# Optimization experiments

Measured on AMD Instinct MI355X. Metric: run time of the kernel, lower is better.

Reference implementation:

```python
import jax, jax.numpy as jnp
import numpy as np

# (multiplicity, dim=2l+1) per irreducible field, for both input and output
RS = [(8, 1), (8, 3), (8, 5)]
SIZE = 3          # conv kernel spatial size
B_EL = 2          # radial basis elements per (i,j) kernel block
EPS = 1e-5


def _se3_bn_conv(x, weight, bases):
    """Training-mode SE3BatchNorm stats fused into dynamic kernel build + conv3d.
    x: (B, C_in, D, H, W); weight: flat (sum mi*mj*b_el,);
    bases[i][j]: (b_el, di, dj, SIZE, SIZE, SIZE).
    """
    B = x.shape[0]
    means = []    # per scalar (d==1) field: (m,)
    scales = []   # per field: (m,) inverse-std factors
    ix = 0
    for m, d in RS:
        field = x[:, ix:ix + m * d].reshape(B, m, d, -1)
        ix += m * d
        if d == 1:
            mean = jax.lax.stop_gradient(field.mean(axis=-1).mean(axis=0).reshape(-1))
            field = field - mean.reshape(1, m, 1, 1)
            means.append(mean)
        # reduce='mean': sum over d, mean over spatial, mean over batch (detached)
        norm = jax.lax.stop_gradient(jnp.sum(field * field, axis=2).mean(axis=-1).mean(axis=0))
        scales.append((norm + EPS) ** -0.5)

    # Build normalized dynamic kernel blocks and compensating bias
    widx = 0
    row_blocks = []
    bias_parts = []
    for i, (mi, di) in enumerate(RS):
        col_blocks = []
        bia = jnp.zeros((mi * di,), x.dtype)
        imean = 0
        for j, (mj, dj) in enumerate(RS):
            basis = bases[i][j]                     # (b, di, dj, s, s, s)
            b = basis.shape[0]
            w = weight[widx:widx + mi * mj * b].reshape(mi, mj, b)
            widx += mi * mj * b
            w = w * scales[j][None, :, None]        # per-input-field BN rescale
            # block: (mi*di, mj*dj, s, s, s)
            block = jnp.einsum('uvb,bdexyz->udvexyz', w, basis)
            col_blocks.append(block.reshape(mi * di, mj * dj, SIZE, SIZE, SIZE))
            if di == 1 and dj == 1:
                mean = means[imean]
                imean += 1
                identity = basis.reshape(b, -1).sum(-1)         # (b,)
                corr = (w.reshape(-1, b) @ identity[:, None]).reshape(mi, mj)
                bia = bia - (corr @ mean[:, None]).reshape(-1)
        row_blocks.append(jnp.concatenate(col_blocks, axis=1))
        bias_parts.append(bia)
    kernel = jnp.concatenate(row_blocks, axis=0)    # (C_out, C_in, s, s, s)
    bias = jnp.concatenate(bias_parts)              # (C_out,)

    out = jax.lax.conv_general_dilated(
        x, kernel, window_strides=(1, 1, 1), padding='VALID',
        dimension_numbers=('NCDHW', 'OIDHW', 'NCDHW'))
    return out + bias[None, :, None, None, None]


def setup_inputs() -> dict:
    key = jax.random.key(0)
    k_x, k_w = jax.random.split(key)
    C = sum(m * d for m, d in RS)  # 72
    x = jax.random.normal(k_x, (8, C, 32, 32, 32), jnp.float32)
    total_w = sum(mi * mj * B_EL for mi, _ in RS for mj, _ in RS)  # 1152
    weight = jax.random.normal(k_w, (total_w,), jnp.float32) * 0.1
    inp = {'x': x, 'weight': weight}
    for i, (mi, di) in enumerate(RS):
        for j, (mj, dj) in enumerate(RS):
            kb = jax.random.fold_in(key, 100 + 10 * i + j)
            inp['basis_{}_{}'.format(i, j)] = jax.random.normal(
                kb, (B_EL, di, dj, SIZE, SIZE, SIZE), jnp.float32) / (SIZE ** 1.5)
    return inp


def reference(x, weight, basis_0_0, basis_0_1, basis_0_2,
              basis_1_0, basis_1_1, basis_1_2,
              basis_2_0, basis_2_1, basis_2_2):
    bases = [[basis_0_0, basis_0_1, basis_0_2],
             [basis_1_0, basis_1_1, basis_1_2],
             [basis_2_0, basis_2_1, basis_2_2]]
    return _se3_bn_conv(x, weight, bases)
```

## Files before the change

### kernel.cpp

```cpp
#include <hip/hip_runtime.h>
#include <hip/hip_fp16.h>
#include <math.h>

#define NCH 72
#define SP  32768
#define NBATCH 8
#define NTOT (NBATCH*SP)

#define WS_SUMX   0
#define WS_SUMSQ  72
#define WS_SCALE  144
#define WS_BIAS   216
#define WS_K      288

#define WS_XH_BYTES 323712
#define XH_ROW   2720
#define XH_PLANE 87040
#define XH_BATCH 2785280

typedef __attribute__((ext_vector_type(8))) _Float16 half8;
typedef __attribute__((ext_vector_type(4))) float float4v;
typedef __attribute__((ext_vector_type(4))) int int4v;

__device__ __forceinline__ void chmap(int c, int& f, int& m, int& d, int& dim) {
  if (c < 8)       { f = 0; m = c;          d = 0;          dim = 1; }
  else if (c < 32) { f = 1; m = (c - 8)/3;  d = (c - 8)%3;  dim = 3; }
  else             { f = 2; m = (c - 32)/5; d = (c - 32)%5; dim = 5; }
}

__global__ __launch_bounds__(256) void prepack_kernel(const float* __restrict__ x,
                                                      float* __restrict__ ws) {
  __shared__ __align__(16) short tile[256 * 88];
  __shared__ float segS[72][3], segQ[72][3];
  const int t    = threadIdx.x;
  const int z    = blockIdx.x >> 1;
  const int half = blockIdx.x & 1;
  const int b    = blockIdx.y;
  ushort* xh = (ushort*)((char*)ws + WS_XH_BYTES);
  const float* xb = x + (size_t)b * NCH * SP + z * 1024 + half * 512;

  const int ci_s = t % 72, seg = t / 72;
  float accS = 0.f, accQ = 0.f;

  for (int c = 0; c < 2; ++c) {
    if (c) __syncthreads();
    #pragma unroll
    for (int cig = 0; cig < 18; ++cig) {
      float v0 = xb[(size_t)(cig*4 + 0) * SP + c * 256 + t];
      float v1 = xb[(size_t)(cig*4 + 1) * SP + c * 256 + t];
      float v2 = xb[(size_t)(cig*4 + 2) * SP + c * 256 + t];
      float v3 = xb[(size_t)(cig*4 + 3) * SP + c * 256 + t];
      short s4[4] = { (short)__half_as_short(__float2half(v0)),
                      (short)__half_as_short(__float2half(v1)),
                      (short)__half_as_short(__float2half(v2)),
                      (short)__half_as_short(__float2half(v3)) };
      *(int2*)&tile[t * 88 + cig * 4] = *(const int2*)s4;
    }
    __syncthreads();
    {
      ushort* gb = xh + (size_t)b * XH_BATCH + (size_t)(z * 32 + (half * 2 + c) * 8) * XH_ROW;
      #pragma unroll
      for (int j = 0; j < 9; ++j) {
        const int4v v = *(const int4v*)&tile[t * 88 + j * 8];
        *(int4v*)(gb + (size_t)(t >> 5) * XH_ROW + j * 272 + (t & 31) * 8) = v;
      }
      {
        const int4v zz = (int4v){0, 0, 0, 0};
        int idx = t;
        *(int4v*)(gb + (size_t)(idx / 34) * XH_ROW + 9 * 272 + (idx % 34) * 8) = zz;
        idx = 256 + t;
        if (idx < 272)
          *(int4v*)(gb + (size_t)(idx / 34) * XH_ROW + 9 * 272 + (idx % 34) * 8) = zz;
      }
    }
    if (seg < 3) {
      const int p0 = seg * 86;
      const int pn = (seg == 2) ? 84 : 86;
      #pragma unroll 4
      for (int i = 0; i < pn; ++i) {
        const float v = __half2float(__short_as_half(tile[(p0 + i) * 88 + ci_s]));
        accS += v; accQ += v * v;
      }
    }
  }
  if (seg < 3) { segS[ci_s][seg] = accS; segQ[ci_s][seg] = accQ; }
  __syncthreads();
  if (t < 144) {
    const int which = t / 72, ci = t % 72;
    const float v = which ? (segQ[ci][0] + segQ[ci][1] + segQ[ci][2])
                          : (segS[ci][0] + segS[ci][1] + segS[ci][2]);
    atomicAdd(&ws[(which ? WS_SUMSQ : WS_SUMX) + ci], v);
  }
}

__global__ __launch_bounds__(256) void build_half_kernel(const float* __restrict__ weight,
    float* __restrict__ ws,
    const float* __restrict__ b00, const float* __restrict__ b01, const float* __restrict__ b02,
    const float* __restrict__ b10, const float* __restrict__ b11, const float* __restrict__ b12,
    const float* __restrict__ b20, const float* __restrict__ b21, const float* __restrict__ b22) {
  const int tid = blockIdx.x * 256 + threadIdx.x;
  const float invN = 1.0f / (float)NTOT;
  if (tid < 315 * 512) {
    const int blk = tid >> 9;
    const int e   = tid & 511;
    const int tap = blk / 35;
    const int r   = blk - tap * 35;
    const int kc  = r / 5, cj = r - (r / 5) * 5;
    const int l   = e >> 3, j = e & 7;
    const int co  = cj * 16 + (l & 15);
    const int kk  = kc * 32 + ((l >> 4) << 3) + j;
    short val = 0;
    if (co < NCH && kk < 216) {
      const int dx = kk / 72, ci = kk - dx * 72;
      int fi, u, dd, di; chmap(co, fi, u, dd, di);
      int fj, v, ee, dj; chmap(ci, fj, v, ee, dj);
      const int s9 = fi * 3 + fj;
      const float* basis = b00;
      if (s9 == 1) basis = b01;
      if (s9 == 2) basis = b02;
      if (s9 == 3) basis = b10;
      if (s9 == 4) basis = b11;
      if (s9 == 5) basis = b12;
      if (s9 == 6) basis = b20;
      if (s9 == 7) basis = b21;
      if (s9 == 8) basis = b22;
      float norm;
      if (ci < 8) {
        float m = ws[WS_SUMX + ci] * invN;
        norm = ws[WS_SUMSQ + ci] * invN - m * m;
      } else if (ci < 32) {
        int m0 = 8 + ((ci - 8) / 3) * 3;
        norm = (ws[WS_SUMSQ+m0] + ws[WS_SUMSQ+m0+1] + ws[WS_SUMSQ+m0+2]) * invN;
      } else {
        int m0 = 32 + ((ci - 32) / 5) * 5;
        norm = (ws[WS_SUMSQ+m0] + ws[WS_SUMSQ+m0+1] + ws[WS_SUMSQ+m0+2]
              + ws[WS_SUMSQ+m0+3] + ws[WS_SUMSQ+m0+4]) * invN;
      }
      const float sc = 1.0f / sqrtf(norm + 1e-5f);
      const float* wp = weight + s9 * 128 + (u * 8 + v) * 2;
      const float w0 = wp[0] * sc, w1 = wp[1] * sc;
      const int t = tap * 3 + dx;
      const float f = w0 * basis[(dd * dj + ee) * 27 + t]
                    + w1 * basis[((di + dd) * dj + ee) * 27 + t];
      val = __half_as_short(__float2half(f));
    }
    ((short*)(ws + WS_K))[tid] = val;
  }
  if (blockIdx.x == 0) {
    __shared__ float s_mean[8], s_scale[8];
    const int c = threadIdx.x;
    if (c < 8) {
      float m = ws[WS_SUMX + c] * invN;
      float norm = ws[WS_SUMSQ + c] * invN - m * m;
      s_mean[c]  = m;
      s_scale[c] = 1.0f / sqrtf(norm + 1e-5f);
    }
    __syncthreads();
    if (c < NCH) {
      float bia = 0.f;
      if (c < 8) {
        float id0 = 0.f, id1 = 0.f;
        #pragma unroll
        for (int t = 0; t < 27; ++t) { id0 += b00[t]; id1 += b00[27 + t]; }
        #pragma unroll
        for (int v = 0; v < 8; ++v) {
          float s  = s_scale[v];
          float w0 = weight[(c*8 + v)*2 + 0] * s;
          float w1 = weight[(c*8 + v)*2 + 1] * s;
          bia -= (w0 * id0 + w1 * id1) * s_mean[v];
        }
      }
      ws[WS_BIAS + c] = bia;
    }
  }
}

__global__ __launch_bounds__(256, 2) void conv_direct(const float* __restrict__ ws,
                                                      float* __restrict__ out) {
  extern __shared__ __align__(16) char Bsm[];

  const int lane = threadIdx.x & 63;
  const int wv   = threadIdx.x >> 6;
  const int lx   = lane & 15;
  const int q    = lane >> 4;
  const int i  = blockIdx.x;
  const int b  = i & 7;
  const int q2 = i >> 3;
  const int yt = q2 & 7;
  const int zp = q2 >> 3;
  const int y  = yt * 4 + wv;
  const int yc = (y > 29) ? 29 : y;
  const int zb = zp * 2;

  const char* xhb = (const char*)ws + WS_XH_BYTES + (size_t)b * (XH_BATCH * 2);
  const char* Kb  = (const char*)(ws + WS_K);
  const float* __restrict__ bias = ws + WS_BIAS;

  const int lb16 = lane * 16;

  int aoffb[7];
  #pragma unroll
  for (int kc = 0; kc < 7; ++kc) {
    const int g = kc * 4 + q;
    aoffb[kc] = ((g >= 27) ? 9 * 544 : (g % 9) * 544 + (g / 9) * 16) + lx * 16;
  }

  float4v acc[2][2][5];
  #pragma unroll
  for (int sz = 0; sz < 2; ++sz)
    #pragma unroll
    for (int s = 0; s < 2; ++s)
      #pragma unroll
      for (int cj = 0; cj < 5; ++cj)
        acc[sz][s][cj] = (float4v){0.f, 0.f, 0.f, 0.f};

#define STAGE(TAP, BUF) {                                                         \
    const char* src_ = Kb + (size_t)(TAP) * 35840;                                \
    char* dst_ = Bsm + (size_t)(BUF) * 35840;                                     \
    _Pragma("unroll")                                                             \
    for (int k = 0; k < 9; ++k) {                                                 \
      const int idx = (int)threadIdx.x + (k << 8);                                \
      if (idx < 2240) {                                                           \
        __builtin_amdgcn_global_load_lds(                                         \
          (const __attribute__((address_space(1))) void*)(src_ + (size_t)idx*16), \
          (__attribute__((address_space(3))) void*)(dst_ + ((k<<8) + (wv<<6))*16),\
          16, 0, 0);                                                              \
      }                                                                           \
    }                                                                             \
  }

#define LOADA(R0, R1, KC, A) {                                                    \
    const int ao_ = aoffb[KC];                                                    \
    A[0] = *(const half8*)((R0) + ao_);                                           \
    A[1] = *(const half8*)((R0) + ao_ + 256);                                     \
    A[2] = *(const half8*)((R1) + ao_);                                           \
    A[3] = *(const half8*)((R1) + ao_ + 256);                                     \
  }

#define BPRE(BC, KC, BQ) {                                                        \
    BQ[0] = *(const half8*)((BC) + ((KC)*5 + 0)*1024 + lb16);                     \
    BQ[1] = *(const half8*)((BC) + ((KC)*5 + 1)*1024 + lb16);                     \
    BQ[2] = *(const half8*)((BC) + ((KC)*5 + 2)*1024 + lb16);                     \
    BQ[3] = *(const half8*)((BC) + ((KC)*5 + 3)*1024 + lb16);                     \
    BQ[4] = *(const half8*)((BC) + ((KC)*5 + 4)*1024 + lb16);                     \
  }

#define MFQ(A, BF, CJ)                                                                         \
    acc[0][0][CJ] = __builtin_amdgcn_mfma_f32_16x16x32_f16(A[0], BF, acc[0][0][CJ], 0,0,0);    \
    acc[0][1][CJ] = __builtin_amdgcn_mfma_f32_16x16x32_f16(A[1], BF, acc[0][1][CJ], 0,0,0);    \
    acc[1][0][CJ] = __builtin_amdgcn_mfma_f32_16x16x32_f16(A[2], BF, acc[1][0][CJ], 0,0,0);    \
    acc[1][1][CJ] = __builtin_amdgcn_mfma_f32_16x16x32_f16(A[3], BF, acc[1][1][CJ], 0,0,0);

#define MFMAG(A, BQ) {                                                            \
    __builtin_amdgcn_s_setprio(1);                                                \
    MFQ(A, BQ[0], 0) MFQ(A, BQ[1], 1) MFQ(A, BQ[2], 2) MFQ(A, BQ[3], 3) MFQ(A, BQ[4], 4) \
    __builtin_amdgcn_s_setprio(0);                                                \
  }

#define TAPBODY(TT, X, Y, Z) {                                                    \
    const int T_  = (TT);                                                         \
    const int dz_ = T_ / 3, dy_ = T_ - 3 * dz_;                                   \
    const char* r0T = xhb + (size_t)(((zb + dz_) * 32) + (yc + dy_)) * (XH_ROW*2);\
    const char* r1T = r0T + (XH_PLANE * 2);                                       \
    const char* Bc  = Bsm + (size_t)(T_ & 1) * 35840;                             \
    BPRE(Bc, 0, Bq0);                                                             \
    if (T_ < 8) STAGE(T_ + 1, ((T_ + 1) & 1));                                    \
    const int Tn_  = (T_ < 8) ? T_ + 1 : T_;                                      \
    const int dzn_ = Tn_ / 3, dyn_ = Tn_ - 3 * dzn_;                              \
    const char* rn0 = xhb + (size_t)(((zb + dzn_) * 32) + (yc + dyn_)) * (XH_ROW*2);\
    const char* rn1 = rn0 + (XH_PLANE * 2);                                       \
    BPRE(Bc, 1, Bq1); LOADA(r0T, r1T, 2, Z);  MFMAG(X, Bq0);                      \
    BPRE(Bc, 2, Bq0); LOADA(r0T, r1T, 3, X);  MFMAG(Y, Bq1);                      \
    BPRE(Bc, 3, Bq1); LOADA(r0T, r1T, 4, Y);  MFMAG(Z, Bq0);                      \
    BPRE(Bc, 4, Bq0); LOADA(r0T, r1T, 5, Z);  MFMAG(X, Bq1);                      \
    BPRE(Bc, 5, Bq1); LOADA(r0T, r1T, 6, X);  MFMAG(Y, Bq0);                      \
    BPRE(Bc, 6, Bq0); if (T_ < 8) LOADA(rn0, rn1, 0, Y);  MFMAG(Z, Bq1);          \
    if (T_ < 8) LOADA(rn0, rn1, 1, Z);  MFMAG(X, Bq0);                            \
    if (T_ < 8) {                                                                 \
      asm volatile("s_waitcnt vmcnt(8)" ::: "memory");                            \
      __builtin_amdgcn_s_barrier();                                               \
    }                                                                             \
  }

  half8 A0[4], A1[4], A2[4], Bq0[5], Bq1[5];

  STAGE(0, 0);
  {
    const char* r0P = xhb + (size_t)((zb * 32) + yc) * (XH_ROW * 2);
    const char* r1P = r0P + (XH_PLANE * 2);
    LOADA(r0P, r1P, 0, A0);
    LOADA(r0P, r1P, 1, A1);
  }
  asm volatile("s_waitcnt vmcnt(8)" ::: "memory");
  __builtin_amdgcn_s_barrier();

  #pragma unroll 1
  for (int s3 = 0; s3 < 9; s3 += 3) {
    TAPBODY(s3 + 0, A0, A1, A2)
    TAPBODY(s3 + 1, A1, A2, A0)
    TAPBODY(s3 + 2, A2, A0, A1)
  }

#undef STAGE
#undef LOADA
#undef BPRE
#undef MFQ
#undef MFMAG
#undef TAPBODY

  if (y < 30) {
    #pragma unroll
    for (int cj = 0; cj < 5; ++cj) {
      const int co = cj * 16 + lx;
      if (co < NCH) {
        const float bv = bias[co];
        #pragma unroll
        for (int sz = 0; sz < 2; ++sz) {
          float* ob = out + ((size_t)(b * NCH + co) * 30 + (zb + sz)) * 900 + y * 30;
          #pragma unroll
          for (int s = 0; s < 2; ++s) {
            const int x0 = s * 16 + q * 4;
            const float4v v = acc[sz][s][cj];
            float2 p0; p0.x = v[0] + bv; p0.y = v[1] + bv;
            *(float2*)(ob + x0) = p0;
            if (x0 + 2 < 30) {
              float2 p1; p1.x = v[2] + bv; p1.y = v[3] + bv;
              *(float2*)(ob + x0 + 2) = p1;
            }
          }
        }
      }
    }
  }
}

extern "C" void kernel_launch(void* const* d_in, const int* in_sizes, int n_in,
                              void* d_out, int out_size, void* d_ws, size_t ws_size,
                              hipStream_t stream) {
  const float* x = (const float*)d_in[0];
  const float* w = (const float*)d_in[1];
  const float* bs[9];
  for (int i = 0; i < 9; ++i) bs[i] = (const float*)d_in[2 + i];
  float* ws  = (float*)d_ws;
  float* out = (float*)d_out;

  hipMemsetAsync(d_ws, 0, 144 * sizeof(float), stream);

  prepack_kernel<<<dim3(64, NBATCH), 256, 0, stream>>>(x, ws);
  build_half_kernel<<<(315 * 512 + 255) / 256, 256, 0, stream>>>(
      w, ws, bs[0], bs[1], bs[2], bs[3], bs[4], bs[5], bs[6], bs[7], bs[8]);
  conv_direct<<<dim3(960), 256, 71680, stream>>>(ws, out);
}
```

Baseline: 234.6 us.

## Halve per-block z tile and drop LDS double buffering to raise occupancy

Each conv block now computes one output z-plane instead of two, which halves the accumulators and A fragments and doubles the grid. The B tap buffer in LDS goes from double to single buffered, so shared memory per block halves and launch bounds ask for four blocks per CU. The cost is that each B tap tile is now loaded from global memory once per z-plane instead of once per two planes, and the cross-tap prefetch pipeline is replaced by a stage-then-barrier pattern with two barriers per tap. Load latency is then hidden by running more resident waves rather than by software pipelining.

Measured after the change: 240.3 us. +2.4%, slower.

```diff
diff --git a/kernel.cpp b/kernel.cpp
--- a/kernel.cpp
+++ b/kernel.cpp
@@ -175,7 +175,7 @@
   }
 }
 
-__global__ __launch_bounds__(256, 2) void conv_direct(const float* __restrict__ ws,
+__global__ __launch_bounds__(256, 4) void conv_direct(const float* __restrict__ ws,
                                                       float* __restrict__ out) {
   extern __shared__ __align__(16) char Bsm[];
 
@@ -190,7 +190,6 @@
   const int zp = q2 >> 3;
   const int y  = yt * 4 + wv;
   const int yc = (y > 29) ? 29 : y;
-  const int zb = zp * 2;
 
   const char* xhb = (const char*)ws + WS_XH_BYTES + (size_t)b * (XH_BATCH * 2);
   const char* Kb  = (const char*)(ws + WS_K);
@@ -205,51 +204,44 @@
     aoffb[kc] = ((g >= 27) ? 9 * 544 : (g % 9) * 544 + (g / 9) * 16) + lx * 16;
   }
 
-  float4v acc[2][2][5];
+  float4v acc[2][5];
   #pragma unroll
-  for (int sz = 0; sz < 2; ++sz)
+  for (int s = 0; s < 2; ++s)
     #pragma unroll
-    for (int s = 0; s < 2; ++s)
-      #pragma unroll
-      for (int cj = 0; cj < 5; ++cj)
-        acc[sz][s][cj] = (float4v){0.f, 0.f, 0.f, 0.f};
-
-#define STAGE(TAP, BUF) {                                                         \
+    for (int cj = 0; cj < 5; ++cj)
+      acc[s][cj] = (float4v){0.f, 0.f, 0.f, 0.f};
+
+#define STAGE(TAP) {                                                              \
     const char* src_ = Kb + (size_t)(TAP) * 35840;                                \
-    char* dst_ = Bsm + (size_t)(BUF) * 35840;                                     \
     _Pragma("unroll")                                                             \
     for (int k = 0; k < 9; ++k) {                                                 \
       const int idx = (int)threadIdx.x + (k << 8);                                \
       if (idx < 2240) {                                                           \
         __builtin_amdgcn_global_load_lds(                                         \
           (const __attribute__((address_space(1))) void*)(src_ + (size_t)idx*16), \
-          (__attribute__((address_space(3))) void*)(dst_ + ((k<<8) + (wv<<6))*16),\
+          (__attribute__((address_space(3))) void*)(Bsm + ((k<<8) + (wv<<6))*16), \
           16, 0, 0);                                                              \
       }                                                                           \
     }                                                                             \
   }
 
-#define LOADA(R0, R1, KC, A) {                                                    \
+#define LOADA(R0, KC, A) {                                                        \
     const int ao_ = aoffb[KC];                                                    \
     A[0] = *(const half8*)((R0) + ao_);                                           \
     A[1] = *(const half8*)((R0) + ao_ + 256);                                     \
-    A[2] = *(const half8*)((R1) + ao_);                                           \
-    A[3] = *(const half8*)((R1) + ao_ + 256);                                     \
-  }
-
-#define BPRE(BC, KC, BQ) {                                                        \
-    BQ[0] = *(const half8*)((BC) + ((KC)*5 + 0)*1024 + lb16);                     \
-    BQ[1] = *(const half8*)((BC) + ((KC)*5 + 1)*1024 + lb16);                     \
-    BQ[2] = *(const half8*)((BC) + ((KC)*5 + 2)*1024 + lb16);                     \
-    BQ[3] = *(const half8*)((BC) + ((KC)*5 + 3)*1024 + lb16);                     \
-    BQ[4] = *(const half8*)((BC) + ((KC)*5 + 4)*1024 + lb16);                     \
-  }
-
-#define MFQ(A, BF, CJ)                                                                         \
-    acc[0][0][CJ] = __builtin_amdgcn_mfma_f32_16x16x32_f16(A[0], BF, acc[0][0][CJ], 0,0,0);    \
-    acc[0][1][CJ] = __builtin_amdgcn_mfma_f32_16x16x32_f16(A[1], BF, acc[0][1][CJ], 0,0,0);    \
-    acc[1][0][CJ] = __builtin_amdgcn_mfma_f32_16x16x32_f16(A[2], BF, acc[1][0][CJ], 0,0,0);    \
-    acc[1][1][CJ] = __builtin_amdgcn_mfma_f32_16x16x32_f16(A[3], BF, acc[1][1][CJ], 0,0,0);
+  }
+
+#define BPRE(KC, BQ) {                                                            \
+    BQ[0] = *(const half8*)(Bsm + ((KC)*5 + 0)*1024 + lb16);                      \
+    BQ[1] = *(const half8*)(Bsm + ((KC)*5 + 1)*1024 + lb16);                      \
+    BQ[2] = *(const half8*)(Bsm + ((KC)*5 + 2)*1024 + lb16);                      \
+    BQ[3] = *(const half8*)(Bsm + ((KC)*5 + 3)*1024 + lb16);                      \
+    BQ[4] = *(const half8*)(Bsm + ((KC)*5 + 4)*1024 + lb16);                      \
+  }
+
+#define MFQ(A, BF, CJ)                                                                      \
+    acc[0][CJ] = __builtin_amdgcn_mfma_f32_16x16x32_f16(A[0], BF, acc[0][CJ], 0,0,0);       \
+    acc[1][CJ] = __builtin_amdgcn_mfma_f32_16x16x32_f16(A[1], BF, acc[1][CJ], 0,0,0);
 
 #define MFMAG(A, BQ) {                                                            \
     __builtin_amdgcn_s_setprio(1);                                                \
@@ -257,48 +249,28 @@
     __builtin_amdgcn_s_setprio(0);                                                \
   }
 
-#define TAPBODY(TT, X, Y, Z) {                                                    \
-    const int T_  = (TT);                                                         \
-    const int dz_ = T_ / 3, dy_ = T_ - 3 * dz_;                                   \
-    const char* r0T = xhb + (size_t)(((zb + dz_) * 32) + (yc + dy_)) * (XH_ROW*2);\
-    const char* r1T = r0T + (XH_PLANE * 2);                                       \
-    const char* Bc  = Bsm + (size_t)(T_ & 1) * 35840;                             \
-    BPRE(Bc, 0, Bq0);                                                             \
-    if (T_ < 8) STAGE(T_ + 1, ((T_ + 1) & 1));                                    \
-    const int Tn_  = (T_ < 8) ? T_ + 1 : T_;                                      \
-    const int dzn_ = Tn_ / 3, dyn_ = Tn_ - 3 * dzn_;                              \
-    const char* rn0 = xhb + (size_t)(((zb + dzn_) * 32) + (yc + dyn_)) * (XH_ROW*2);\
-    const char* rn1 = rn0 + (XH_PLANE * 2);                                       \
-    BPRE(Bc, 1, Bq1); LOADA(r0T, r1T, 2, Z);  MFMAG(X, Bq0);                      \
-    BPRE(Bc, 2, Bq0); LOADA(r0T, r1T, 3, X);  MFMAG(Y, Bq1);                      \
-    BPRE(Bc, 3, Bq1); LOADA(r0T, r1T, 4, Y);  MFMAG(Z, Bq0);                      \
-    BPRE(Bc, 4, Bq0); LOADA(r0T, r1T, 5, Z);  MFMAG(X, Bq1);                      \
-    BPRE(Bc, 5, Bq1); LOADA(r0T, r1T, 6, X);  MFMAG(Y, Bq0);                      \
-    BPRE(Bc, 6, Bq0); if (T_ < 8) LOADA(rn0, rn1, 0, Y);  MFMAG(Z, Bq1);          \
-    if (T_ < 8) LOADA(rn0, rn1, 1, Z);  MFMAG(X, Bq0);                            \
-    if (T_ < 8) {                                                                 \
-      asm volatile("s_waitcnt vmcnt(8)" ::: "memory");                            \
-      __builtin_amdgcn_s_barrier();                                               \
-    }                                                                             \
-  }
-
-  half8 A0[4], A1[4], A2[4], Bq0[5], Bq1[5];
-
-  STAGE(0, 0);
-  {
-    const char* r0P = xhb + (size_t)((zb * 32) + yc) * (XH_ROW * 2);
-    const char* r1P = r0P + (XH_PLANE * 2);
-    LOADA(r0P, r1P, 0, A0);
-    LOADA(r0P, r1P, 1, A1);
-  }
-  asm volatile("s_waitcnt vmcnt(8)" ::: "memory");
-  __builtin_amdgcn_s_barrier();
+  half8 AA[2], AB[2], AC[2], Bq0[5], Bq1[5];
 
   #pragma unroll 1
-  for (int s3 = 0; s3 < 9; s3 += 3) {
-    TAPBODY(s3 + 0, A0, A1, A2)
-    TAPBODY(s3 + 1, A1, A2, A0)
-    TAPBODY(s3 + 2, A2, A0, A1)
+  for (int tap = 0; tap < 9; ++tap) {
+    const int dz_ = tap / 3, dy_ = tap - 3 * dz_;
+    const char* r0T = xhb + (size_t)(((zp + dz_) * 32) + (yc + dy_)) * (XH_ROW * 2);
+
+    if (tap) __builtin_amdgcn_s_barrier();
+    STAGE(tap);
+    LOADA(r0T, 0, AA);
+    LOADA(r0T, 1, AB);
+    asm volatile("s_waitcnt vmcnt(4)" ::: "memory");
+    __builtin_amdgcn_s_barrier();
+
+    BPRE(0, Bq0);
+    BPRE(1, Bq1); LOADA(r0T, 2, AC); MFMAG(AA, Bq0);
+    BPRE(2, Bq0); LOADA(r0T, 3, AA); MFMAG(AB, Bq1);
+    BPRE(3, Bq1); LOADA(r0T, 4, AB); MFMAG(AC, Bq0);
+    BPRE(4, Bq0); LOADA(r0T, 5, AC); MFMAG(AA, Bq1);
+    BPRE(5, Bq1); LOADA(r0T, 6, AA); MFMAG(AB, Bq0);
+    BPRE(6, Bq0);                    MFMAG(AC, Bq1);
+                                     MFMAG(AA, Bq0);
   }
 
 #undef STAGE
@@ -306,7 +278,6 @@
 #undef BPRE
 #undef MFQ
 #undef MFMAG
-#undef TAPBODY
 
   if (y < 30) {
     #pragma unroll
@@ -314,19 +285,16 @@
       const int co = cj * 16 + lx;
       if (co < NCH) {
         const float bv = bias[co];
+        float* ob = out + ((size_t)(b * NCH + co) * 30 + zp) * 900 + y * 30;
         #pragma unroll
-        for (int sz = 0; sz < 2; ++sz) {
-          float* ob = out + ((size_t)(b * NCH + co) * 30 + (zb + sz)) * 900 + y * 30;
-          #pragma unroll
-          for (int s = 0; s < 2; ++s) {
-            const int x0 = s * 16 + q * 4;
-            const float4v v = acc[sz][s][cj];
-            float2 p0; p0.x = v[0] + bv; p0.y = v[1] + bv;
-            *(float2*)(ob + x0) = p0;
-            if (x0 + 2 < 30) {
-              float2 p1; p1.x = v[2] + bv; p1.y = v[3] + bv;
-              *(float2*)(ob + x0 + 2) = p1;
-            }
+        for (int s = 0; s < 2; ++s) {
+          const int x0 = s * 16 + q * 4;
+          const float4v v = acc[s][cj];
+          float2 p0; p0.x = v[0] + bv; p0.y = v[1] + bv;
+          *(float2*)(ob + x0) = p0;
+          if (x0 + 2 < 30) {
+            float2 p1; p1.x = v[2] + bv; p1.y = v[3] + bv;
+            *(float2*)(ob + x0 + 2) = p1;
           }
         }
       }
@@ -349,5 +317,5 @@
   prepack_kernel<<<dim3(64, NBATCH), 256, 0, stream>>>(x, ws);
   build_half_kernel<<<(315 * 512 + 255) / 256, 256, 0, stream>>>(
       w, ws, bs[0], bs[1], bs[2], bs[3], bs[4], bs[5], bs[6], bs[7], bs[8]);
-  conv_direct<<<dim3(960), 256, 71680, stream>>>(ws, out);
-}
+  conv_direct<<<dim3(1920), 256, 35840, stream>>>(ws, out);
+}
```
